# Optimization experiments

Measured on AMD Instinct MI355X. Metric: run time of the kernel, lower is better.

## Reference

```python
import jax, jax.numpy as jnp
import numpy as np

N, E, DIN, ED, H, C = 50000, 800000, 128, 16, 4, 128
HC = H * C
SLOPE = 0.2


def gat_conv(x, ei_src, ei_dst, ea, W, a_src, a_dst, We, a_e, b):
    # x: [N, din]; ea: [E, ed] (self-loops already appended by caller)
    n = x.shape[0]
    h = (x @ W).reshape(n, H, C)                       # [N,H,C]
    al_src = (h * a_src).sum(-1)                       # [N,H]
    al_dst = (h * a_dst).sum(-1)                       # [N,H]
    e = (ea @ We).reshape(-1, H, C)                    # [E,H,C]
    al_e = (e * a_e).sum(-1)                           # [E,H]
    alpha = al_src[ei_src] + al_dst[ei_dst] + al_e     # [E,H]
    alpha = jnp.where(alpha > 0, alpha, SLOPE * alpha)  # LeakyReLU(0.2)
    # per-destination-node segment softmax (stable)
    amax = jax.ops.segment_max(alpha, ei_dst, num_segments=n)
    amax = jnp.where(jnp.isfinite(amax), amax, 0.0)
    ex = jnp.exp(alpha - amax[ei_dst])
    den = jax.ops.segment_sum(ex, ei_dst, num_segments=n)
    alpha = ex / (den[ei_dst] + 1e-16)                 # [E,H]
    msg = h[ei_src] * alpha[:, :, None]                # [E,H,C]
    out = jax.ops.segment_sum(msg, ei_dst, num_segments=n)  # [N,H,C]
    return out.reshape(n, HC) + b


def setup_inputs() -> dict:
    key = jax.random.key(0)
    ks = jax.random.split(key, 16)
    s = 0.05
    inp = {
        "x": jax.random.normal(ks[0], (N, DIN), jnp.float32),
        "edge_index": jax.random.randint(ks[1], (2, E), 0, N, jnp.int64),
        "edge_features": jax.random.normal(ks[2], (E, ED), jnp.float32),
        # layer 1 params
        "W1": jax.random.normal(ks[3], (DIN, HC), jnp.float32) * s,
        "att_src1": jax.random.normal(ks[4], (H, C), jnp.float32) * s,
        "att_dst1": jax.random.normal(ks[5], (H, C), jnp.float32) * s,
        "lin_e1": jax.random.normal(ks[6], (ED, HC), jnp.float32) * s,
        "att_e1": jax.random.normal(ks[7], (H, C), jnp.float32) * s,
        "b1": jnp.zeros((HC,), jnp.float32),
        # layer 2 params
        "W2": jax.random.normal(ks[8], (HC, HC), jnp.float32) * s,
        "att_src2": jax.random.normal(ks[9], (H, C), jnp.float32) * s,
        "att_dst2": jax.random.normal(ks[10], (H, C), jnp.float32) * s,
        "lin_e2": jax.random.normal(ks[11], (ED, HC), jnp.float32) * s,
        "att_e2": jax.random.normal(ks[12], (H, C), jnp.float32) * s,
        "b2": jnp.zeros((HC,), jnp.float32),
    }
    return inp


def reference(x, edge_index, edge_features,
              W1, att_src1, att_dst1, lin_e1, att_e1, b1,
              W2, att_src2, att_dst2, lin_e2, att_e2, b2):
    # add self-loops once (PyG default: add_self_loops=True, edge_attr fill='mean')
    loop = jnp.arange(N, dtype=edge_index.dtype)
    ei_src = jnp.concatenate([edge_index[0], loop])
    ei_dst = jnp.concatenate([edge_index[1], loop])
    mean_ea = edge_features.mean(0)
    ea = jnp.concatenate([edge_features, jnp.broadcast_to(mean_ea, (N, ED))], axis=0)

    h = gat_conv(x, ei_src, ei_dst, ea, W1, att_src1, att_dst1, lin_e1, att_e1, b1)
    h = jax.nn.elu(h)
    h = gat_conv(h, ei_src, ei_dst, ea, W2, att_src2, att_dst2, lin_e2, att_e2, b2)
    return jax.nn.elu(h)
```

## Files before the change

kernel.cpp:

```cpp
#include <hip/hip_runtime.h>
#include <math.h>

#define NNODE 50000
#define NEDGE 800000
#define DINv  128
#define EDv   16
#define NHv   4
#define CHv   128
#define HCv   512
#define SLOPEv 0.2f
#define MEANBLK 512
#define CONVN (NNODE * DINv / 4)
#define NCOUNT ((NEDGE + 255) / 256)

typedef __attribute__((ext_vector_type(8))) short bf16x8;
typedef __attribute__((ext_vector_type(4))) float f32x4;
typedef __attribute__((ext_vector_type(4))) unsigned u32x4;
typedef __attribute__((address_space(3))) unsigned lds_u32;
typedef const __attribute__((address_space(1))) unsigned glb_u32;

__device__ __forceinline__ ushort f2b(float f) {
  unsigned u = __float_as_uint(f);
  u += 0x7FFF + ((u >> 16) & 1);
  return (ushort)(u >> 16);
}
__device__ __forceinline__ float blo(unsigned u) { return __uint_as_float(u << 16); }
__device__ __forceinline__ float bhi(unsigned u) { return __uint_as_float(u & 0xffff0000u); }

__device__ __forceinline__ void nt_store16(void* p, unsigned a, unsigned b, unsigned c,
                                           unsigned d) {
  u32x4 t = {a, b, c, d};
  __builtin_nontemporal_store(t, (u32x4*)p);
}

__global__ void detect_kernel(const int* __restrict__ ei, int* __restrict__ flag) {
  __shared__ int bad;
  if (threadIdx.x == 0) bad = 0;
  __syncthreads();
  for (int i = threadIdx.x; i < 2048; i += 256)
    if (ei[2 * i + 1] != 0) bad = 1;
  __syncthreads();
  if (threadIdx.x == 0) flag[0] = bad ? 0 : 1;
}

__device__ __forceinline__ int load_idx(const int* __restrict__ ei, int e, int row, int wide) {
  if (wide) return ei[2 * ((size_t)row * NEDGE + e)];
  return ei[(size_t)row * NEDGE + e];
}

__global__ void prep_misc_kernel(const int* __restrict__ ei, const int* __restrict__ flag,
                                 int* __restrict__ deg,
                                 const float* __restrict__ ea, float* __restrict__ partials,
                                 const float* __restrict__ We1, const float* __restrict__ ae1,
                                 const float* __restrict__ We2, const float* __restrict__ ae2,
                                 float* __restrict__ v1, float* __restrict__ v2,
                                 const float* __restrict__ x, const float* __restrict__ W1,
                                 const float* __restrict__ W2, ushort* __restrict__ xb,
                                 ushort* __restrict__ Bt1, ushort* __restrict__ Bt2) {
  int b = blockIdx.x;
  if (b < NCOUNT) {
    int e = b * 256 + threadIdx.x;
    if (e < NEDGE) {
      int w = flag[0];
      atomicAdd(&deg[load_idx(ei, e, 1, w)], 1);
    }
    return;
  }
  b -= NCOUNT;
  if (b < MEANBLK) {
    float acc[EDv];
#pragma unroll
    for (int d = 0; d < EDv; d++) acc[d] = 0.f;
    const int stride = MEANBLK * 256;
    for (int r = b * 256 + threadIdx.x; r < NEDGE; r += stride) {
      const float4* p = (const float4*)(ea + (size_t)r * EDv);
#pragma unroll
      for (int q = 0; q < 4; q++) {
        float4 v = p[q];
        acc[q * 4 + 0] += v.x; acc[q * 4 + 1] += v.y;
        acc[q * 4 + 2] += v.z; acc[q * 4 + 3] += v.w;
      }
    }
    __shared__ float red[4][EDv];
    int wid = threadIdx.x >> 6, lane = threadIdx.x & 63;
#pragma unroll
    for (int d = 0; d < EDv; d++) {
      float v = acc[d];
      for (int off = 32; off; off >>= 1) v += __shfl_down(v, off, 64);
      if (lane == 0) red[wid][d] = v;
    }
    __syncthreads();
    if (threadIdx.x < EDv) {
      float v = red[0][threadIdx.x] + red[1][threadIdx.x] + red[2][threadIdx.x] +
                red[3][threadIdx.x];
      partials[b * EDv + threadIdx.x] = v;
    }
  } else if (b == MEANBLK) {
    int t = threadIdx.x;
    if (t < 128) {
      int layer = t >> 6, u = t & 63;
      int d = u >> 2, h = u & 3;
      const float* We = layer ? We2 : We1;
      const float* ae = layer ? ae2 : ae1;
      float s = 0.f;
      for (int c = 0; c < CHv; c++) s += We[(size_t)d * HCv + h * CHv + c] * ae[h * CHv + c];
      (layer ? v2 : v1)[d * 4 + h] = s;
    }
  } else {
    int i = (b - MEANBLK - 1) * 256 + threadIdx.x;
    if (i < CONVN) {
      float4 v = ((const float4*)x)[i];
      ushort4 o;
      o.x = f2b(v.x); o.y = f2b(v.y); o.z = f2b(v.z); o.w = f2b(v.w);
      ((ushort4*)xb)[i] = o;
    } else if (i < CONVN + DINv * HCv) {
      int idx = i - CONVN;
      int k = idx >> 9, n = idx & (HCv - 1);
      Bt1[(size_t)n * DINv + k] = f2b(W1[idx]);
    } else if (i < CONVN + DINv * HCv + HCv * HCv) {
      int idx = i - CONVN - DINv * HCv;
      int k = idx >> 9, n = idx & (HCv - 1);
      Bt2[(size_t)n * HCv + k] = f2b(W2[idx]);
    }
  }
}

__global__ __launch_bounds__(1024) void scan_fold_kernel(
    const int* __restrict__ deg, int* __restrict__ row_ptr,
    const float* __restrict__ partials, const float* __restrict__ v1,
    const float* __restrict__ v2, float* __restrict__ loop1, float* __restrict__ loop2) {
  int tid = threadIdx.x;
  if (blockIdx.x == 0) {
    __shared__ int wsum[16];
    int wid = tid >> 6, lane = tid & 63;
    int carry = 0;
    for (int base = 0; base < NNODE; base += 4096) {
      int idx = base + tid * 4;
      int4 x = make_int4(0, 0, 0, 0);
      if (idx < NNODE) x = *(const int4*)(deg + idx);
      int t0 = x.x, t1 = t0 + x.y, t2 = t1 + x.z, t3 = t2 + x.w;
      int v = t3;
#pragma unroll
      for (int off = 1; off < 64; off <<= 1) {
        int t = __shfl_up(v, off, 64);
        if (lane >= off) v += t;
      }
      if (lane == 63) wsum[wid] = v;
      __syncthreads();
      if (wid == 0) {
        int s = (lane < 16) ? wsum[lane] : 0;
#pragma unroll
        for (int off = 1; off < 16; off <<= 1) {
          int t = __shfl_up(s, off, 64);
          if (lane >= off) s += t;
        }
        if (lane < 16) wsum[lane] = s;
      }
      __syncthreads();
      int woff = wid ? wsum[wid - 1] : 0;
      int excl = carry + woff + v - t3;
      if (idx < NNODE) {
        int4 o = make_int4(excl, excl + t0, excl + t1, excl + t2);
        *(int4*)(row_ptr + idx) = o;
      }
      carry += wsum[15];
      __syncthreads();
    }
    if (tid == 0) row_ptr[NNODE] = carry;
  } else {
    __shared__ float buf[1024];
    __shared__ float ms[16];
    int d = tid & 15, r0 = tid >> 4;
    float v = 0.f;
    for (int r = r0; r < MEANBLK; r += 64) v += partials[r * EDv + d];
    buf[tid] = v;
    __syncthreads();
#pragma unroll
    for (int off = 32; off >= 1; off >>= 1) {
      if (r0 < off) buf[tid] += buf[tid + off * 16];
      __syncthreads();
    }
    if (tid < 16) ms[tid] = buf[tid] * (1.0f / NEDGE);
    __syncthreads();
    if (tid < 8) {
      const float* vv = (tid >> 2) ? v2 : v1;
      int h = tid & 3;
      float a = 0.f;
      for (int d2 = 0; d2 < EDv; d2++) a += ms[d2] * vv[d2 * 4 + h];
      ((tid >> 2) ? loop2 : loop1)[h] = a;
    }
  }
}

__global__ void apre1_kernel(const int* __restrict__ eid_sorted, const int* __restrict__ ei,
                             const int* __restrict__ flag,
                             const float* __restrict__ ea, const float* __restrict__ al_src,
                             const float* __restrict__ v1, const float* __restrict__ v2,
                             float* __restrict__ ap1, float* __restrict__ ale2s,
                             int* __restrict__ src_sorted) {
  __shared__ float sv1[64], sv2[64];
  if (threadIdx.x < 64) sv1[threadIdx.x] = v1[threadIdx.x];
  else if (threadIdx.x < 128) sv2[threadIdx.x - 64] = v2[threadIdx.x - 64];
  __syncthreads();
  int p = blockIdx.x * 256 + threadIdx.x;
  if (p >= NEDGE) return;
  int e = eid_sorted[p];
  int w = flag[0];
  int s = load_idx(ei, e, 0, w);
  const float4* pr = (const float4*)(ea + (size_t)e * EDv);
  float row[16];
  *(float4*)&row[0] = pr[0]; *(float4*)&row[4] = pr[1];
  *(float4*)&row[8] = pr[2]; *(float4*)&row[12] = pr[3];
  float a0 = 0, a1 = 0, a2 = 0, a3 = 0;
  float b0 = 0, b1 = 0, b2 = 0, b3 = 0;
#pragma unroll
  for (int d = 0; d < 16; d++) {
    a0 += row[d] * sv1[d * 4 + 0];
    a1 += row[d] * sv1[d * 4 + 1];
    a2 += row[d] * sv1[d * 4 + 2];
    a3 += row[d] * sv1[d * 4 + 3];
    b0 += row[d] * sv2[d * 4 + 0];
    b1 += row[d] * sv2[d * 4 + 1];
    b2 += row[d] * sv2[d * 4 + 2];
    b3 += row[d] * sv2[d * 4 + 3];
  }
  float4 as = ((const float4*)al_src)[s];
  ((float4*)ap1)[p] = make_float4(as.x + a0, as.y + a1, as.z + a2, as.w + a3);
  ((float4*)ale2s)[p] = make_float4(b0, b1, b2, b3);
  src_sorted[p] = s;
}

__global__ __launch_bounds__(256) void gemm_mfma_kernel(const ushort* __restrict__ A,
                                                        const ushort* __restrict__ Bt,
                                                        ushort* __restrict__ C, int M, int K,
                                                        const float* __restrict__ a_src,
                                                        const float* __restrict__ a_dst,
                                                        float* __restrict__ al_src,
                                                        float* __restrict__ al_dst,
                                                        int ngemm,
                                                        const int* __restrict__ ei,
                                                        const int* __restrict__ flag,
                                                        const int* __restrict__ row_ptr,
                                                        int* __restrict__ cursor,
                                                        int* __restrict__ eid_sorted) {
  int j = blockIdx.x;
  if (j >= ngemm) {
    int e = (j - ngemm) * 256 + threadIdx.x;
    if (e < NEDGE) {
      int w = flag[0];
      int d0 = load_idx(ei, e, 1, w);
      int p = row_ptr[d0] + atomicAdd(&cursor[d0], 1);
      eid_sorted[p] = e;
    }
    return;
  }

  __shared__ ushort As[8][128][8];
  __shared__ ushort Bs[8][128][8];
  __shared__ float ssa[128], ssd[128];
  __shared__ float rsum[2][128][2];
  int tid = threadIdx.x;
  int wid = tid >> 6, lane = tid & 63;

  int q = ngemm >> 3, rem = ngemm & 7;
  int xcd = j & 7, idx = j >> 3;
  int d = (xcd < rem) ? xcd * (q + 1) + idx : rem * (q + 1) + (xcd - rem) * q + idx;
  int rb = (d >> 2) * 128, cb = (d & 3) * 128;
  int hblk = cb >> 7;

  int wm = (wid >> 1) * 64, wn = (wid & 1) * 64;
  int lr = lane & 15, lq = lane >> 4;

  if (tid < 128) { ssa[tid] = a_src[cb + tid]; ssd[tid] = a_dst[cb + tid]; }

  f32x4 acc[4][4];
#pragma unroll
  for (int i = 0; i < 4; i++)
#pragma unroll
    for (int jx = 0; jx < 4; jx++) acc[i][jx] = (f32x4){0.f, 0.f, 0.f, 0.f};

  ushort* AsF = &As[0][0][0];
  ushort* BsF = &Bs[0][0][0];

  for (int k0 = 0; k0 < K; k0 += 64) {
#pragma unroll
    for (int s = 0; s < 4; s++) {
      int c = s * 256 + tid;
      int kq = c >> 7, m = c & 127;
      int row = rb + m; if (row >= M) row = M - 1;
      const ushort* gA = A + (size_t)row * K + k0 + kq * 8;
      __builtin_amdgcn_global_load_lds((glb_u32*)gA, (lds_u32*)(AsF + (size_t)c * 8), 16, 0, 0);
    }
#pragma unroll
    for (int s = 0; s < 4; s++) {
      int c = s * 256 + tid;
      int kq = c >> 7, n = c & 127;
      const ushort* gB = Bt + (size_t)(cb + n) * K + k0 + kq * 8;
      __builtin_amdgcn_global_load_lds((glb_u32*)gB, (lds_u32*)(BsF + (size_t)c * 8), 16, 0, 0);
    }
    __syncthreads();
#pragma unroll
    for (int hh = 0; hh < 2; hh++) {
      bf16x8 af[4], bfr[4];
#pragma unroll
      for (int i = 0; i < 4; i++) {
        af[i]  = *(const bf16x8*)&As[hh * 4 + lq][wm + i * 16 + lr][0];
        bfr[i] = *(const bf16x8*)&Bs[hh * 4 + lq][wn + i * 16 + lr][0];
      }
#pragma unroll
      for (int i = 0; i < 4; i++)
#pragma unroll
        for (int jx = 0; jx < 4; jx++)
          acc[i][jx] = __builtin_amdgcn_mfma_f32_16x16x32_bf16(af[i], bfr[jx], acc[i][jx], 0, 0, 0);
    }
    __syncthreads();
  }

#pragma unroll
  for (int i = 0; i < 4; i++) {
    int rbase = rb + wm + i * 16 + lq * 4;
#pragma unroll
    for (int jx = 0; jx < 4; jx++) {
      int col = cb + wn + jx * 16 + lr;
#pragma unroll
      for (int r = 0; r < 4; r++) {
        int row = rbase + r;
        if (row < M) C[(size_t)row * HCv + col] = f2b(acc[i][jx][r]);
      }
    }
  }

  float sa[4], sd[4];
#pragma unroll
  for (int jx = 0; jx < 4; jx++) {
    int c = wn + jx * 16 + lr;
    sa[jx] = ssa[c]; sd[jx] = ssd[c];
  }
#pragma unroll
  for (int i = 0; i < 4; i++) {
#pragma unroll
    for (int r = 0; r < 4; r++) {
      float s1 = 0.f, s2 = 0.f;
#pragma unroll
      for (int jx = 0; jx < 4; jx++) {
        s1 = fmaf(acc[i][jx][r], sa[jx], s1);
        s2 = fmaf(acc[i][jx][r], sd[jx], s2);
      }
#pragma unroll
      for (int off = 1; off < 16; off <<= 1) {
        s1 += __shfl_xor(s1, off, 16);
        s2 += __shfl_xor(s2, off, 16);
      }
      if (lr == 0) {
        int row = wm + i * 16 + lq * 4 + r;
        rsum[0][row][wn >> 6] = s1;
        rsum[1][row][wn >> 6] = s2;
      }
    }
  }
  __syncthreads();
  if (tid < 128) {
    int row = rb + tid;
    if (row < M) {
      al_src[(size_t)row * 4 + hblk] = rsum[0][tid][0] + rsum[0][tid][1];
      al_dst[(size_t)row * 4 + hblk] = rsum[1][tid][0] + rsum[1][tid][1];
    }
  }
}

__device__ __forceinline__ void fma8(float* acc, float w, uint4 u) {
  acc[0] = fmaf(w, blo(u.x), acc[0]);
  acc[1] = fmaf(w, bhi(u.x), acc[1]);
  acc[2] = fmaf(w, blo(u.y), acc[2]);
  acc[3] = fmaf(w, bhi(u.y), acc[3]);
  acc[4] = fmaf(w, blo(u.z), acc[4]);
  acc[5] = fmaf(w, bhi(u.z), acc[5]);
  acc[6] = fmaf(w, blo(u.w), acc[6]);
  acc[7] = fmaf(w, bhi(u.w), acc[7]);
}

__global__ __launch_bounds__(256) void node_kernel(
    const ushort* __restrict__ hb, const float* __restrict__ al_src,
    const float* __restrict__ al_dst, const float* __restrict__ ap,
    const float* __restrict__ loop_al_e, const int* __restrict__ row_ptr,
    const int* __restrict__ src_sorted, const float* __restrict__ bias,
    const float* __restrict__ asrc_g,
    float* __restrict__ outf, ushort* __restrict__ outb) {
  int wid = threadIdx.x >> 6, lane = threadIdx.x & 63;
  int n = blockIdx.x * 4 + wid;
  if (n >= NNODE) return;
  int base = row_ptr[n];
  int deg = row_ptr[n + 1] - base;
  int h = lane >> 4;
  int jj = lane & 15;

  float aldh = al_dst[(size_t)n * 4 + h];
  float a0 = al_src[(size_t)n * 4 + h] + aldh + loop_al_e[h];
  float alph = a0 > 0.f ? a0 : SLOPEv * a0;
  float wl = __expf(alph);

  uint4 uself = *((const uint4*)(hb + ((size_t)n << 9)) + lane);

  float acc[8];
#pragma unroll
  for (int q = 0; q < 8; q++) acc[q] = 0.f;
  float den = 0.f;

  for (int cs = 0; cs < deg; cs += 16) {
    int cl = min(16, deg - cs);
    float w = 0.f;
    int sv = 0;
    if (jj < cl) {
      int p = base + cs + jj;
      sv = src_sorted[p];
      float a = ap[(size_t)p * 4 + h] + aldh;
      if (asrc_g) a += asrc_g[(size_t)sv * 4 + h];
      a = a > 0.f ? a : SLOPEv * a;
      w = __expf(a);
      den += w;
    }
    int cl4 = (cl + 3) & ~3;
    for (int j0 = 0; j0 < cl4; j0 += 4) {
      int s0 = __shfl(sv, j0 + 0, 16);
      int s1 = __shfl(sv, j0 + 1, 16);
      int s2 = __shfl(sv, j0 + 2, 16);
      int s3 = __shfl(sv, j0 + 3, 16);
      float w0 = __shfl(w, j0 + 0, 16);
      float w1 = __shfl(w, j0 + 1, 16);
      float w2 = __shfl(w, j0 + 2, 16);
      float w3 = __shfl(w, j0 + 3, 16);
      uint4 u0 = *((const uint4*)(hb + ((size_t)s0 << 9)) + lane);
      uint4 u1 = *((const uint4*)(hb + ((size_t)s1 << 9)) + lane);
      uint4 u2 = *((const uint4*)(hb + ((size_t)s2 << 9)) + lane);
      uint4 u3 = *((const uint4*)(hb + ((size_t)s3 << 9)) + lane);
      fma8(acc, w0, u0);
      fma8(acc, w1, u1);
      fma8(acc, w2, u2);
      fma8(acc, w3, u3);
    }
  }

  fma8(acc, wl, uself);

#pragma unroll
  for (int off = 8; off; off >>= 1) den += __shfl_xor(den, off, 16);
  den += wl;
  float rden = 1.f / (den + 1e-16f);

  const float4* bp = (const float4*)(bias + lane * 8);
  float4 b0 = bp[0], b1 = bp[1];
  float bv[8] = {b0.x, b0.y, b0.z, b0.w, b1.x, b1.y, b1.z, b1.w};
  float r[8];
#pragma unroll
  for (int q = 0; q < 8; q++) {
    float t = acc[q] * rden + bv[q];
    r[q] = t > 0.f ? t : expm1f(t);
  }
  if (outf) {
    float* op = outf + (size_t)n * HCv + lane * 8;
    nt_store16(op, __float_as_uint(r[0]), __float_as_uint(r[1]),
               __float_as_uint(r[2]), __float_as_uint(r[3]));
    nt_store16(op + 4, __float_as_uint(r[4]), __float_as_uint(r[5]),
               __float_as_uint(r[6]), __float_as_uint(r[7]));
  }
  if (outb) {
    uint4 o;
    o.x = (unsigned)f2b(r[0]) | ((unsigned)f2b(r[1]) << 16);
    o.y = (unsigned)f2b(r[2]) | ((unsigned)f2b(r[3]) << 16);
    o.z = (unsigned)f2b(r[4]) | ((unsigned)f2b(r[5]) << 16);
    o.w = (unsigned)f2b(r[6]) | ((unsigned)f2b(r[7]) << 16);
    ((uint4*)(outb + (size_t)n * HCv))[lane] = o;
  }
}

static inline char* take(char*& p, size_t bytes) {
  char* r = p;
  p += (bytes + 255) & ~(size_t)255;
  return r;
}

extern "C" void kernel_launch(void* const* d_in, const int* in_sizes, int n_in,
                              void* d_out, int out_size, void* d_ws, size_t ws_size,
                              hipStream_t stream) {
  (void)in_sizes; (void)n_in; (void)out_size; (void)ws_size;
  const float* x   = (const float*)d_in[0];
  const int*   ei  = (const int*)d_in[1];
  const float* ea  = (const float*)d_in[2];
  const float* W1  = (const float*)d_in[3];
  const float* as1 = (const float*)d_in[4];
  const float* ad1 = (const float*)d_in[5];
  const float* We1 = (const float*)d_in[6];
  const float* ae1 = (const float*)d_in[7];
  const float* b1  = (const float*)d_in[8];
  const float* W2  = (const float*)d_in[9];
  const float* as2 = (const float*)d_in[10];
  const float* ad2 = (const float*)d_in[11];
  const float* We2 = (const float*)d_in[12];
  const float* ae2 = (const float*)d_in[13];
  const float* b2  = (const float*)d_in[14];
  float* out = (float*)d_out;

  char* p = (char*)d_ws;
  ushort* hb        = (ushort*)take(p, (size_t)NNODE * HCv * 2);
  float* al_src     = (float*)take(p, (size_t)NNODE * 4 * 4);
  float* al_dst     = (float*)take(p, (size_t)NNODE * 4 * 4);
  float* ap         = (float*)take(p, (size_t)NEDGE * 4 * 4);
  float* ale2s      = (float*)take(p, (size_t)NEDGE * 4 * 4);
  int*   src_sorted = (int*)take(p, (size_t)NEDGE * 4);
  int*   eid_sorted = (int*)take(p, (size_t)NEDGE * 4);
  int*   row_ptr    = (int*)take(p, (size_t)(NNODE + 1) * 4);
  float* partials   = (float*)take(p, (size_t)MEANBLK * EDv * 4);
  ushort* Bt1       = (ushort*)take(p, (size_t)HCv * DINv * 2);
  ushort* Bt2       = (ushort*)take(p, (size_t)HCv * HCv * 2);
  char* zero_begin = p;
  int*   deg        = (int*)take(p, (size_t)NNODE * 4);
  int*   cursor     = (int*)take(p, (size_t)NNODE * 4);
  size_t zero_len = (size_t)(p - zero_begin);
  float* v1         = (float*)take(p, 64 * 4);
  float* v2         = (float*)take(p, 64 * 4);
  float* loop1      = (float*)take(p, 4 * 4);
  float* loop2      = (float*)take(p, 4 * 4);
  int*   flag       = (int*)take(p, 4);

  ushort* xb  = (ushort*)d_out;
  ushort* h1b = (ushort*)((char*)d_out + (size_t)16 * 1024 * 1024);

  hipMemsetAsync(zero_begin, 0, zero_len, stream);

  const int NGEMM = 4 * ((NNODE + 127) / 128);

  detect_kernel<<<1, 256, 0, stream>>>(ei, flag);
  prep_misc_kernel<<<NCOUNT + MEANBLK + 1 + (CONVN + DINv * HCv + HCv * HCv + 255) / 256, 256,
                     0, stream>>>(ei, flag, deg, ea, partials, We1, ae1, We2, ae2, v1, v2,
                                  x, W1, W2, xb, Bt1, Bt2);
  scan_fold_kernel<<<2, 1024, 0, stream>>>(deg, row_ptr, partials, v1, v2, loop1, loop2);

  gemm_mfma_kernel<<<NGEMM + NCOUNT, 256, 0, stream>>>(
      xb, Bt1, hb, NNODE, DINv, as1, ad1, al_src, al_dst,
      NGEMM, ei, flag, row_ptr, cursor, eid_sorted);
  apre1_kernel<<<(NEDGE + 255) / 256, 256, 0, stream>>>(eid_sorted, ei, flag, ea, al_src,
                                                        v1, v2, ap, ale2s, src_sorted);
  node_kernel<<<(NNODE + 3) / 4, 256, 0, stream>>>(hb, al_src, al_dst, ap, loop1, row_ptr,
                                                   src_sorted, b1, (const float*)nullptr,
                                                   (float*)nullptr, h1b);

  gemm_mfma_kernel<<<NGEMM, 256, 0, stream>>>(
      h1b, Bt2, hb, NNODE, HCv, as2, ad2, al_src, al_dst,
      NGEMM, ei, flag, row_ptr, cursor, eid_sorted);
  node_kernel<<<(NNODE + 3) / 4, 256, 0, stream>>>(hb, al_src, al_dst, ale2s, loop2, row_ptr,
                                                   src_sorted, b2, al_src,
                                                   out, (ushort*)nullptr);
}
```

Measured before the change: 679.6 us.

## Fuse edge attention precompute into layer-1 node aggregation kernel

Removes the separate apre1 kernel and computes the per-edge edge-feature attention terms, source index and layer-2 edge term inside the layer-1 node kernel, each lane handling one head. This eliminates a kernel launch and the write/read of the ap buffer, at the cost of redundant reads of edge features across four head lanes and more work on the aggregation critical path. It also widens the gather unroll from 4 to 8 neighbors to raise memory-level parallelism, and switches the bf16 output store to a non-temporal store.

```diff
diff --git a/kernel.cpp b/kernel.cpp
--- a/kernel.cpp
+++ b/kernel.cpp
@@ -190,44 +190,6 @@
       ((tid >> 2) ? loop2 : loop1)[h] = a;
     }
   }
-}
-
-__global__ void apre1_kernel(const int* __restrict__ eid_sorted, const int* __restrict__ ei,
-                             const int* __restrict__ flag,
-                             const float* __restrict__ ea, const float* __restrict__ al_src,
-                             const float* __restrict__ v1, const float* __restrict__ v2,
-                             float* __restrict__ ap1, float* __restrict__ ale2s,
-                             int* __restrict__ src_sorted) {
-  __shared__ float sv1[64], sv2[64];
-  if (threadIdx.x < 64) sv1[threadIdx.x] = v1[threadIdx.x];
-  else if (threadIdx.x < 128) sv2[threadIdx.x - 64] = v2[threadIdx.x - 64];
-  __syncthreads();
-  int p = blockIdx.x * 256 + threadIdx.x;
-  if (p >= NEDGE) return;
-  int e = eid_sorted[p];
-  int w = flag[0];
-  int s = load_idx(ei, e, 0, w);
-  const float4* pr = (const float4*)(ea + (size_t)e * EDv);
-  float row[16];
-  *(float4*)&row[0] = pr[0]; *(float4*)&row[4] = pr[1];
-  *(float4*)&row[8] = pr[2]; *(float4*)&row[12] = pr[3];
-  float a0 = 0, a1 = 0, a2 = 0, a3 = 0;
-  float b0 = 0, b1 = 0, b2 = 0, b3 = 0;
-#pragma unroll
-  for (int d = 0; d < 16; d++) {
-    a0 += row[d] * sv1[d * 4 + 0];
-    a1 += row[d] * sv1[d * 4 + 1];
-    a2 += row[d] * sv1[d * 4 + 2];
-    a3 += row[d] * sv1[d * 4 + 3];
-    b0 += row[d] * sv2[d * 4 + 0];
-    b1 += row[d] * sv2[d * 4 + 1];
-    b2 += row[d] * sv2[d * 4 + 2];
-    b3 += row[d] * sv2[d * 4 + 3];
-  }
-  float4 as = ((const float4*)al_src)[s];
-  ((float4*)ap1)[p] = make_float4(as.x + a0, as.y + a1, as.z + a2, as.w + a3);
-  ((float4*)ale2s)[p] = make_float4(b0, b1, b2, b3);
-  src_sorted[p] = s;
 }
 
 __global__ __launch_bounds__(256) void gemm_mfma_kernel(const ushort* __restrict__ A,
@@ -381,11 +343,20 @@
 
 __global__ __launch_bounds__(256) void node_kernel(
     const ushort* __restrict__ hb, const float* __restrict__ al_src,
-    const float* __restrict__ al_dst, const float* __restrict__ ap,
-    const float* __restrict__ loop_al_e, const int* __restrict__ row_ptr,
-    const int* __restrict__ src_sorted, const float* __restrict__ bias,
-    const float* __restrict__ asrc_g,
-    float* __restrict__ outf, ushort* __restrict__ outb) {
+    const float* __restrict__ al_dst, const float* __restrict__ loop_al_e,
+    const int* __restrict__ row_ptr, const float* __restrict__ bias,
+    const int* __restrict__ eid_sorted, const int* __restrict__ ei,
+    const int* __restrict__ flag, const float* __restrict__ ea,
+    const float* __restrict__ v1, const float* __restrict__ v2,
+    int* __restrict__ src_sorted, float* __restrict__ ale2s,
+    int mode, float* __restrict__ outf, ushort* __restrict__ outb) {
+  __shared__ float sv1[64], sv2[64];
+  if (mode == 0) {
+    if (threadIdx.x < 64) sv1[threadIdx.x] = v1[threadIdx.x];
+    else if (threadIdx.x < 128) sv2[threadIdx.x - 64] = v2[threadIdx.x - 64];
+  }
+  __syncthreads();
+
   int wid = threadIdx.x >> 6, lane = threadIdx.x & 63;
   int n = blockIdx.x * 4 + wid;
   if (n >= NNODE) return;
@@ -393,6 +364,7 @@
   int deg = row_ptr[n + 1] - base;
   int h = lane >> 4;
   int jj = lane & 15;
+  int wide = flag[0];
 
   float aldh = al_dst[(size_t)n * 4 + h];
   float a0 = al_src[(size_t)n * 4 + h] + aldh + loop_al_e[h];
@@ -412,31 +384,66 @@
     int sv = 0;
     if (jj < cl) {
       int p = base + cs + jj;
-      sv = src_sorted[p];
-      float a = ap[(size_t)p * 4 + h] + aldh;
-      if (asrc_g) a += asrc_g[(size_t)sv * 4 + h];
+      float a;
+      if (mode == 0) {
+        int e = eid_sorted[p];
+        int s = load_idx(ei, e, 0, wide);
+        sv = s;
+        const float4* pr = (const float4*)(ea + (size_t)e * EDv);
+        float row[16];
+        *(float4*)&row[0] = pr[0]; *(float4*)&row[4] = pr[1];
+        *(float4*)&row[8] = pr[2]; *(float4*)&row[12] = pr[3];
+        float a1 = 0.f, b2 = 0.f;
+#pragma unroll
+        for (int d = 0; d < 16; d++) {
+          a1 = fmaf(row[d], sv1[d * 4 + h], a1);
+          b2 = fmaf(row[d], sv2[d * 4 + h], b2);
+        }
+        ale2s[(size_t)p * 4 + h] = b2;
+        if (h == 0) src_sorted[p] = s;
+        a = al_src[(size_t)s * 4 + h] + a1 + aldh;
+      } else {
+        sv = src_sorted[p];
+        a = ale2s[(size_t)p * 4 + h] + al_src[(size_t)sv * 4 + h] + aldh;
+      }
       a = a > 0.f ? a : SLOPEv * a;
       w = __expf(a);
       den += w;
     }
-    int cl4 = (cl + 3) & ~3;
-    for (int j0 = 0; j0 < cl4; j0 += 4) {
+    int cl8 = (cl + 7) & ~7;
+    for (int j0 = 0; j0 < cl8; j0 += 8) {
       int s0 = __shfl(sv, j0 + 0, 16);
       int s1 = __shfl(sv, j0 + 1, 16);
       int s2 = __shfl(sv, j0 + 2, 16);
       int s3 = __shfl(sv, j0 + 3, 16);
+      int s4 = __shfl(sv, j0 + 4, 16);
+      int s5 = __shfl(sv, j0 + 5, 16);
+      int s6 = __shfl(sv, j0 + 6, 16);
+      int s7 = __shfl(sv, j0 + 7, 16);
       float w0 = __shfl(w, j0 + 0, 16);
       float w1 = __shfl(w, j0 + 1, 16);
       float w2 = __shfl(w, j0 + 2, 16);
       float w3 = __shfl(w, j0 + 3, 16);
+      float w4 = __shfl(w, j0 + 4, 16);
+      float w5 = __shfl(w, j0 + 5, 16);
+      float w6 = __shfl(w, j0 + 6, 16);
+      float w7 = __shfl(w, j0 + 7, 16);
       uint4 u0 = *((const uint4*)(hb + ((size_t)s0 << 9)) + lane);
       uint4 u1 = *((const uint4*)(hb + ((size_t)s1 << 9)) + lane);
       uint4 u2 = *((const uint4*)(hb + ((size_t)s2 << 9)) + lane);
       uint4 u3 = *((const uint4*)(hb + ((size_t)s3 << 9)) + lane);
+      uint4 u4 = *((const uint4*)(hb + ((size_t)s4 << 9)) + lane);
+      uint4 u5 = *((const uint4*)(hb + ((size_t)s5 << 9)) + lane);
+      uint4 u6 = *((const uint4*)(hb + ((size_t)s6 << 9)) + lane);
+      uint4 u7 = *((const uint4*)(hb + ((size_t)s7 << 9)) + lane);
       fma8(acc, w0, u0);
       fma8(acc, w1, u1);
       fma8(acc, w2, u2);
       fma8(acc, w3, u3);
+      fma8(acc, w4, u4);
+      fma8(acc, w5, u5);
+      fma8(acc, w6, u6);
+      fma8(acc, w7, u7);
     }
   }
 
@@ -464,12 +471,11 @@
                __float_as_uint(r[6]), __float_as_uint(r[7]));
   }
   if (outb) {
-    uint4 o;
-    o.x = (unsigned)f2b(r[0]) | ((unsigned)f2b(r[1]) << 16);
-    o.y = (unsigned)f2b(r[2]) | ((unsigned)f2b(r[3]) << 16);
-    o.z = (unsigned)f2b(r[4]) | ((unsigned)f2b(r[5]) << 16);
-    o.w = (unsigned)f2b(r[6]) | ((unsigned)f2b(r[7]) << 16);
-    ((uint4*)(outb + (size_t)n * HCv))[lane] = o;
+    nt_store16(outb + (size_t)n * HCv + lane * 8,
+               (unsigned)f2b(r[0]) | ((unsigned)f2b(r[1]) << 16),
+               (unsigned)f2b(r[2]) | ((unsigned)f2b(r[3]) << 16),
+               (unsigned)f2b(r[4]) | ((unsigned)f2b(r[5]) << 16),
+               (unsigned)f2b(r[6]) | ((unsigned)f2b(r[7]) << 16));
   }
 }
 
@@ -504,7 +510,6 @@
   ushort* hb        = (ushort*)take(p, (size_t)NNODE * HCv * 2);
   float* al_src     = (float*)take(p, (size_t)NNODE * 4 * 4);
   float* al_dst     = (float*)take(p, (size_t)NNODE * 4 * 4);
-  float* ap         = (float*)take(p, (size_t)NEDGE * 4 * 4);
   float* ale2s      = (float*)take(p, (size_t)NEDGE * 4 * 4);
   int*   src_sorted = (int*)take(p, (size_t)NEDGE * 4);
   int*   eid_sorted = (int*)take(p, (size_t)NEDGE * 4);
@@ -538,16 +543,16 @@
   gemm_mfma_kernel<<<NGEMM + NCOUNT, 256, 0, stream>>>(
       xb, Bt1, hb, NNODE, DINv, as1, ad1, al_src, al_dst,
       NGEMM, ei, flag, row_ptr, cursor, eid_sorted);
-  apre1_kernel<<<(NEDGE + 255) / 256, 256, 0, stream>>>(eid_sorted, ei, flag, ea, al_src,
-                                                        v1, v2, ap, ale2s, src_sorted);
-  node_kernel<<<(NNODE + 3) / 4, 256, 0, stream>>>(hb, al_src, al_dst, ap, loop1, row_ptr,
-                                                   src_sorted, b1, (const float*)nullptr,
-                                                   (float*)nullptr, h1b);
+  node_kernel<<<(NNODE + 3) / 4, 256, 0, stream>>>(
+      hb, al_src, al_dst, loop1, row_ptr, b1,
+      eid_sorted, ei, flag, ea, v1, v2, src_sorted, ale2s,
+      0, (float*)nullptr, h1b);
 
   gemm_mfma_kernel<<<NGEMM, 256, 0, stream>>>(
       h1b, Bt2, hb, NNODE, HCv, as2, ad2, al_src, al_dst,
       NGEMM, ei, flag, row_ptr, cursor, eid_sorted);
-  node_kernel<<<(NNODE + 3) / 4, 256, 0, stream>>>(hb, al_src, al_dst, ale2s, loop2, row_ptr,
-                                                   src_sorted, b2, al_src,
-                                                   out, (ushort*)nullptr);
-}
+  node_kernel<<<(NNODE + 3) / 4, 256, 0, stream>>>(
+      hb, al_src, al_dst, loop2, row_ptr, b2,
+      eid_sorted, ei, flag, ea, v1, v2, src_sorted, ale2s,
+      1, out, (ushort*)nullptr);
+}
```

Result: no change. 687.5 us (+1.2%).

## Fuse edge attention precompute into GEMM scatter blocks and drop apre1 kernel

Applied to the files above, without the earlier changes.

The edge-feature attention projections for both layers are now computed in the edge-scatter blocks of the first GEMM launch and stored by original edge id. Each sorted slot stores (edge id, source) as an int2, which removes the separate apre1 kernel and its extra pass over the edge data. In exchange, node_kernel now gathers al_src by source and ale by edge id in random order instead of reading a presorted contiguous array. Layer-1 bf16 output writes switch to non-temporal stores.

```diff
diff --git a/kernel.cpp b/kernel.cpp
--- a/kernel.cpp
+++ b/kernel.cpp
@@ -192,44 +192,6 @@
   }
 }
 
-__global__ void apre1_kernel(const int* __restrict__ eid_sorted, const int* __restrict__ ei,
-                             const int* __restrict__ flag,
-                             const float* __restrict__ ea, const float* __restrict__ al_src,
-                             const float* __restrict__ v1, const float* __restrict__ v2,
-                             float* __restrict__ ap1, float* __restrict__ ale2s,
-                             int* __restrict__ src_sorted) {
-  __shared__ float sv1[64], sv2[64];
-  if (threadIdx.x < 64) sv1[threadIdx.x] = v1[threadIdx.x];
-  else if (threadIdx.x < 128) sv2[threadIdx.x - 64] = v2[threadIdx.x - 64];
-  __syncthreads();
-  int p = blockIdx.x * 256 + threadIdx.x;
-  if (p >= NEDGE) return;
-  int e = eid_sorted[p];
-  int w = flag[0];
-  int s = load_idx(ei, e, 0, w);
-  const float4* pr = (const float4*)(ea + (size_t)e * EDv);
-  float row[16];
-  *(float4*)&row[0] = pr[0]; *(float4*)&row[4] = pr[1];
-  *(float4*)&row[8] = pr[2]; *(float4*)&row[12] = pr[3];
-  float a0 = 0, a1 = 0, a2 = 0, a3 = 0;
-  float b0 = 0, b1 = 0, b2 = 0, b3 = 0;
-#pragma unroll
-  for (int d = 0; d < 16; d++) {
-    a0 += row[d] * sv1[d * 4 + 0];
-    a1 += row[d] * sv1[d * 4 + 1];
-    a2 += row[d] * sv1[d * 4 + 2];
-    a3 += row[d] * sv1[d * 4 + 3];
-    b0 += row[d] * sv2[d * 4 + 0];
-    b1 += row[d] * sv2[d * 4 + 1];
-    b2 += row[d] * sv2[d * 4 + 2];
-    b3 += row[d] * sv2[d * 4 + 3];
-  }
-  float4 as = ((const float4*)al_src)[s];
-  ((float4*)ap1)[p] = make_float4(as.x + a0, as.y + a1, as.z + a2, as.w + a3);
-  ((float4*)ale2s)[p] = make_float4(b0, b1, b2, b3);
-  src_sorted[p] = s;
-}
-
 __global__ __launch_bounds__(256) void gemm_mfma_kernel(const ushort* __restrict__ A,
                                                         const ushort* __restrict__ Bt,
                                                         ushort* __restrict__ C, int M, int K,
@@ -242,15 +204,44 @@
                                                         const int* __restrict__ flag,
                                                         const int* __restrict__ row_ptr,
                                                         int* __restrict__ cursor,
-                                                        int* __restrict__ eid_sorted) {
+                                                        int2* __restrict__ es_sorted,
+                                                        const float* __restrict__ ea,
+                                                        const float* __restrict__ v1g,
+                                                        const float* __restrict__ v2g,
+                                                        float* __restrict__ ale1,
+                                                        float* __restrict__ ale2) {
   int j = blockIdx.x;
   if (j >= ngemm) {
+    __shared__ float sv1[64], sv2[64];
+    if (threadIdx.x < 64) sv1[threadIdx.x] = v1g[threadIdx.x];
+    else if (threadIdx.x < 128) sv2[threadIdx.x - 64] = v2g[threadIdx.x - 64];
+    __syncthreads();
     int e = (j - ngemm) * 256 + threadIdx.x;
     if (e < NEDGE) {
       int w = flag[0];
       int d0 = load_idx(ei, e, 1, w);
+      int s  = load_idx(ei, e, 0, w);
       int p = row_ptr[d0] + atomicAdd(&cursor[d0], 1);
-      eid_sorted[p] = e;
+      es_sorted[p] = make_int2(e, s);
+      const float4* pr = (const float4*)(ea + (size_t)e * EDv);
+      float row[16];
+      *(float4*)&row[0] = pr[0]; *(float4*)&row[4] = pr[1];
+      *(float4*)&row[8] = pr[2]; *(float4*)&row[12] = pr[3];
+      float a0 = 0, a1 = 0, a2 = 0, a3 = 0;
+      float b0 = 0, b1 = 0, b2 = 0, b3 = 0;
+#pragma unroll
+      for (int d = 0; d < 16; d++) {
+        a0 += row[d] * sv1[d * 4 + 0];
+        a1 += row[d] * sv1[d * 4 + 1];
+        a2 += row[d] * sv1[d * 4 + 2];
+        a3 += row[d] * sv1[d * 4 + 3];
+        b0 += row[d] * sv2[d * 4 + 0];
+        b1 += row[d] * sv2[d * 4 + 1];
+        b2 += row[d] * sv2[d * 4 + 2];
+        b3 += row[d] * sv2[d * 4 + 3];
+      }
+      ((float4*)ale1)[e] = make_float4(a0, a1, a2, a3);
+      ((float4*)ale2)[e] = make_float4(b0, b1, b2, b3);
     }
     return;
   }
@@ -381,10 +372,9 @@
 
 __global__ __launch_bounds__(256) void node_kernel(
     const ushort* __restrict__ hb, const float* __restrict__ al_src,
-    const float* __restrict__ al_dst, const float* __restrict__ ap,
+    const float* __restrict__ al_dst, const float* __restrict__ ale,
     const float* __restrict__ loop_al_e, const int* __restrict__ row_ptr,
-    const int* __restrict__ src_sorted, const float* __restrict__ bias,
-    const float* __restrict__ asrc_g,
+    const int2* __restrict__ es_sorted, const float* __restrict__ bias,
     float* __restrict__ outf, ushort* __restrict__ outb) {
   int wid = threadIdx.x >> 6, lane = threadIdx.x & 63;
   int n = blockIdx.x * 4 + wid;
@@ -412,9 +402,11 @@
     int sv = 0;
     if (jj < cl) {
       int p = base + cs + jj;
-      sv = src_sorted[p];
-      float a = ap[(size_t)p * 4 + h] + aldh;
-      if (asrc_g) a += asrc_g[(size_t)sv * 4 + h];
+      int2 es = es_sorted[p];
+      sv = es.y;
+      float a = al_src[(size_t)sv * 4 + h]
+              + ale[(size_t)es.x * 4 + h]
+              + aldh;
       a = a > 0.f ? a : SLOPEv * a;
       w = __expf(a);
       den += w;
@@ -464,12 +456,11 @@
                __float_as_uint(r[6]), __float_as_uint(r[7]));
   }
   if (outb) {
-    uint4 o;
-    o.x = (unsigned)f2b(r[0]) | ((unsigned)f2b(r[1]) << 16);
-    o.y = (unsigned)f2b(r[2]) | ((unsigned)f2b(r[3]) << 16);
-    o.z = (unsigned)f2b(r[4]) | ((unsigned)f2b(r[5]) << 16);
-    o.w = (unsigned)f2b(r[6]) | ((unsigned)f2b(r[7]) << 16);
-    ((uint4*)(outb + (size_t)n * HCv))[lane] = o;
+    nt_store16(outb + (size_t)n * HCv + lane * 8,
+               (unsigned)f2b(r[0]) | ((unsigned)f2b(r[1]) << 16),
+               (unsigned)f2b(r[2]) | ((unsigned)f2b(r[3]) << 16),
+               (unsigned)f2b(r[4]) | ((unsigned)f2b(r[5]) << 16),
+               (unsigned)f2b(r[6]) | ((unsigned)f2b(r[7]) << 16));
   }
 }
 
@@ -504,10 +495,9 @@
   ushort* hb        = (ushort*)take(p, (size_t)NNODE * HCv * 2);
   float* al_src     = (float*)take(p, (size_t)NNODE * 4 * 4);
   float* al_dst     = (float*)take(p, (size_t)NNODE * 4 * 4);
-  float* ap         = (float*)take(p, (size_t)NEDGE * 4 * 4);
-  float* ale2s      = (float*)take(p, (size_t)NEDGE * 4 * 4);
-  int*   src_sorted = (int*)take(p, (size_t)NEDGE * 4);
-  int*   eid_sorted = (int*)take(p, (size_t)NEDGE * 4);
+  float* ale1       = (float*)take(p, (size_t)NEDGE * 4 * 4);
+  float* ale2       = (float*)take(p, (size_t)NEDGE * 4 * 4);
+  int2*  es_sorted  = (int2*)take(p, (size_t)NEDGE * 8);
   int*   row_ptr    = (int*)take(p, (size_t)(NNODE + 1) * 4);
   float* partials   = (float*)take(p, (size_t)MEANBLK * EDv * 4);
   ushort* Bt1       = (ushort*)take(p, (size_t)HCv * DINv * 2);
@@ -537,17 +527,15 @@
 
   gemm_mfma_kernel<<<NGEMM + NCOUNT, 256, 0, stream>>>(
       xb, Bt1, hb, NNODE, DINv, as1, ad1, al_src, al_dst,
-      NGEMM, ei, flag, row_ptr, cursor, eid_sorted);
-  apre1_kernel<<<(NEDGE + 255) / 256, 256, 0, stream>>>(eid_sorted, ei, flag, ea, al_src,
-                                                        v1, v2, ap, ale2s, src_sorted);
-  node_kernel<<<(NNODE + 3) / 4, 256, 0, stream>>>(hb, al_src, al_dst, ap, loop1, row_ptr,
-                                                   src_sorted, b1, (const float*)nullptr,
-                                                   (float*)nullptr, h1b);
+      NGEMM, ei, flag, row_ptr, cursor, es_sorted, ea, v1, v2, ale1, ale2);
+  node_kernel<<<(NNODE + 3) / 4, 256, 0, stream>>>(
+      hb, al_src, al_dst, ale1, loop1, row_ptr, es_sorted, b1,
+      (float*)nullptr, h1b);
 
   gemm_mfma_kernel<<<NGEMM, 256, 0, stream>>>(
       h1b, Bt2, hb, NNODE, HCv, as2, ad2, al_src, al_dst,
-      NGEMM, ei, flag, row_ptr, cursor, eid_sorted);
-  node_kernel<<<(NNODE + 3) / 4, 256, 0, stream>>>(hb, al_src, al_dst, ale2s, loop2, row_ptr,
-                                                   src_sorted, b2, al_src,
-                                                   out, (ushort*)nullptr);
-}
+      NGEMM, ei, flag, row_ptr, cursor, es_sorted, ea, v1, v2, ale1, ale2);
+  node_kernel<<<(NNODE + 3) / 4, 256, 0, stream>>>(
+      hb, al_src, al_dst, ale2, loop2, row_ptr, es_sorted, b2,
+      out, (ushort*)nullptr);
+}
```

After: 695.0 us. +2.3%, slower.
